# Kernel optimization log

Measured on AMD Instinct MI355X. Metric: run time of the kernel, lower is better.

The kernel has to match this reference:

```python
import jax, jax.numpy as jnp
import numpy as np

C = 512
H_HEADS = 8  # self-attn heads (num_heads) and cross-attn heads (n_heads), both 8


def _self_attn(x, Wq, Wkv):
    # x: [B,N,C]; shared (ModuleParallel) linear weights, qkv_bias=False
    B, N, _ = x.shape
    h, d = H_HEADS, C // H_HEADS
    q = (x @ Wq.T).reshape(B, N, h, d).transpose(0, 2, 1, 3)          # [B,h,N,d]
    kv = (x @ Wkv.T).reshape(B, N, 2, h, d).transpose(2, 0, 3, 1, 4)  # [2,B,h,N,d]
    k, v = kv[0], kv[1]
    attn = jax.nn.softmax(jnp.einsum('bhnd,bhmd->bhnm', q, k) * (d ** -0.5), axis=-1)
    y = jnp.einsum('bhnm,bhmd->bhnd', attn, v).transpose(0, 2, 1, 3).reshape(B, N, C)
    return y


def _judger(y_self, y_other, Wj1, bj1, Wj2, bj2):
    # Mlp_2(2C->C->C) with exact GELU, then softmax over channel dim
    hdn = jax.nn.gelu(jnp.concatenate([y_self, y_other], axis=-1) @ Wj1.T + bj1, approximate=False)
    return jax.nn.softmax(hdn @ Wj2.T + bj2, axis=-1)


def _cross_attn(yq, ykv, kn_row, vn_row, Win, bin_, Wout, bout, rel):
    # Vectorized form of the per-sample loop: each token is a seq-len-1 query
    # attending over 2 keys: [noise_k + yq, yq * relation_score].
    B, N, _ = yq.shape
    h, d = H_HEADS, C // H_HEADS
    qw, kw, vw = Win[:C], Win[C:2 * C], Win[2 * C:]
    bq, bk, bv = bin_[:C], bin_[C:2 * C], bin_[2 * C:]
    k_in = jnp.stack([kn_row + yq, yq * rel], axis=-2)   # [B,N,2,C]
    v_in = jnp.stack([vn_row + yq, ykv], axis=-2)        # [B,N,2,C]
    qp = (yq @ qw.T + bq).reshape(B, N, h, d)
    kp = (k_in @ kw.T + bk).reshape(B, N, 2, h, d)
    vp = (v_in @ vw.T + bv).reshape(B, N, 2, h, d)
    scores = jnp.einsum('bnhd,bnkhd->bnhk', qp, kp) * (d ** -0.5)
    w = jax.nn.softmax(scores, axis=-1)
    o = jnp.einsum('bnhk,bnkhd->bnhd', w, vp).reshape(B, N, C)
    return o @ Wout.T + bout


def setup_inputs() -> dict:
    key = jax.random.key(0)
    ks = jax.random.split(key, 16)
    B, N = 8, 1024
    s = 0.02
    inp = {
        'x0': jax.random.normal(ks[0], (B, N, C), jnp.float32),
        'x1': jax.random.normal(ks[1], (B, N, C), jnp.float32),
        'H': 32, 'W': 32,
        'Wq': jax.random.normal(ks[2], (C, C), jnp.float32) * s,
        'Wkv': jax.random.normal(ks[3], (2 * C, C), jnp.float32) * s,
        'Wj1': jax.random.normal(ks[4], (C, 2 * C), jnp.float32) * s,
        'bj1': jnp.zeros((C,), jnp.float32),
        'Wj2': jax.random.normal(ks[5], (C, C), jnp.float32) * s,
        'bj2': jnp.zeros((C,), jnp.float32),
        'kn': jax.random.normal(ks[6], (2, C), jnp.float32),
        'vn': jax.random.normal(ks[7], (2, C), jnp.float32),
        'Wc0_in': jax.random.normal(ks[8], (3 * C, C), jnp.float32) * s,
        'bc0_in': jnp.zeros((3 * C,), jnp.float32),
        'Wc0_out': jax.random.normal(ks[9], (C, C), jnp.float32) * s,
        'bc0_out': jnp.zeros((C,), jnp.float32),
        'Wc1_in': jax.random.normal(ks[10], (3 * C, C), jnp.float32) * s,
        'bc1_in': jnp.zeros((3 * C,), jnp.float32),
        'Wc1_out': jax.random.normal(ks[11], (C, C), jnp.float32) * s,
        'bc1_out': jnp.zeros((C,), jnp.float32),
        'Wp': jax.random.normal(ks[12], (C, C), jnp.float32) * s,
        'bp': jnp.zeros((C,), jnp.float32),
    }
    return inp


def reference(x0, x1, H, W, Wq, Wkv, Wj1, bj1, Wj2, bj2, kn, vn,
              Wc0_in, bc0_in, Wc0_out, bc0_out, Wc1_in, bc1_in, Wc1_out, bc1_out,
              Wp, bp):
    # Dual self-attention (shared q/kv projections across modalities, sr_ratio=1)
    y0 = _self_attn(x0, Wq, Wkv)
    y1 = _self_attn(x1, Wq, Wkv)
    # Noise-augmented relation-gated cross-attention (vectorized over batch)
    rel0 = _judger(y0, y1, Wj1, bj1, Wj2, bj2)
    rel1 = _judger(y1, y0, Wj1, bj1, Wj2, bj2)
    new0 = y0 + _cross_attn(y0, y1, kn[0], vn[0], Wc0_in, bc0_in, Wc0_out, bc0_out, rel0)
    new1 = y1 + _cross_attn(y1, y0, kn[1], vn[1], Wc1_in, bc1_in, Wc1_out, bc1_out, rel1)
    out0 = new0 @ Wp.T + bp
    out1 = new1 @ Wp.T + bp
    return jnp.stack([out0, out1])  # [2,B,N,C]
```

## Files before the change

kernel.cpp:

```cpp
#include <hip/hip_runtime.h>

typedef unsigned short u16;
typedef u16 u16x8 __attribute__((ext_vector_type(8)));
typedef __bf16 bf16x8 __attribute__((ext_vector_type(8)));
typedef __bf16 bf16x2 __attribute__((ext_vector_type(2)));
typedef float f32x4 __attribute__((ext_vector_type(4)));

__device__ __forceinline__ float b2f(u16 h) {
  union { unsigned u; float f; } x; x.u = ((unsigned)h) << 16; return x.f;
}
__device__ __forceinline__ u16 f2b(float f) {
  union { float f; unsigned u; } x; x.f = f;
  unsigned r = x.u + 0x7FFFu + ((x.u >> 16) & 1u);
  return (u16)(r >> 16);
}
__device__ __forceinline__ f32x4 mfma16(bf16x8 a, bf16x8 b, f32x4 c) {
  return __builtin_amdgcn_mfma_f32_16x16x32_bf16(a, b, c, 0, 0, 0);
}
__device__ __forceinline__ void gload16(const void* g, void* l) {
  __builtin_amdgcn_global_load_lds(
      (const __attribute__((address_space(1))) void*)g,
      (__attribute__((address_space(3))) void*)l, 16, 0, 0);
}
#define WAITV4 asm volatile("s_waitcnt vmcnt(4)" ::: "memory")
#define WAITV0 asm volatile("s_waitcnt vmcnt(0)" ::: "memory")
#define WAITL0 asm volatile("s_waitcnt lgkmcnt(0)" ::: "memory")
#define BARRIER asm volatile("s_barrier" ::: "memory")

__global__ __launch_bounds__(256) void xcvt_k(const float* __restrict__ x0,
                                              const float* __restrict__ x1,
                                              u16* __restrict__ out) {
  int b = blockIdx.x;
  const float* src = (b < 4096) ? x0 : x1;
  u16* dst = out + (b < 4096 ? 0 : 4194304);
  int i = (b & 4095) * 1024 + threadIdx.x * 4;
  float4 v = *(const float4*)&src[i];
  dst[i + 0] = f2b(v.x); dst[i + 1] = f2b(v.y);
  dst[i + 2] = f2b(v.z); dst[i + 3] = f2b(v.w);
}

__global__ __launch_bounds__(256) void wcvt_k(
    const float* __restrict__ wq, const float* __restrict__ wkv,
    const float* __restrict__ wj1, const float* __restrict__ wj2,
    const float* __restrict__ wci0, const float* __restrict__ wci1,
    const float* __restrict__ wp, u16* __restrict__ wsb) {
  int b = blockIdx.x; const float* src; size_t doff; int lb;
  if      (b < 256)  { src = wq;   doff = 0;       lb = b; }
  else if (b < 768)  { src = wkv;  doff = 262144;  lb = b - 256; }
  else if (b < 1280) { src = wj1;  doff = 786432;  lb = b - 768; }
  else if (b < 1536) { src = wj2;  doff = 1310720; lb = b - 1280; }
  else if (b < 2304) { src = wci0; doff = 1572864; lb = b - 1536; }
  else if (b < 3072) { src = wci1; doff = 2359296; lb = b - 2304; }
  else               { src = wp;   doff = 3145728; lb = b - 3072; }
  int i = lb * 1024 + threadIdx.x * 4;
  float4 v = *(const float4*)&src[i];
  u16* dst = wsb + doff + i;
  u16 c0 = f2b(v.x), c1 = f2b(v.y), c2 = f2b(v.z), c3 = f2b(v.w);
  dst[0] = c0; dst[1] = c1; dst[2] = c2; dst[3] = c3;
  if (b >= 3072) {
    int row = i >> 9, col = i & 511;
    u16* f0 = wsb + 3932160 + (size_t)row * 1024 + col;
    u16* f1 = wsb + 4456448 + (size_t)row * 1024 + col;
    f0[0] = c0; f0[1] = c1; f0[2] = c2; f0[3] = c3;
    f1[0] = c0; f1[1] = c1; f1[2] = c2; f1[3] = c3;
  }
}

__global__ __launch_bounds__(256) void tcvt_k(const float* __restrict__ w0,
                                              const float* __restrict__ w1,
                                              u16* __restrict__ o0,
                                              u16* __restrict__ o1) {
  __shared__ u16 t[64][65];
  const int b = blockIdx.x;
  const float* src = (b & 64) ? w1 : w0;
  u16* dst = (b & 64) ? o1 : o0;
  const int r0 = ((b >> 3) & 7) * 64, c0 = (b & 7) * 64;
  const int tid = threadIdx.x;
#pragma unroll
  for (int i = 0; i < 16; i++) {
    int idx = tid + i * 256;
    int r = idx >> 6, c = idx & 63;
    t[r][c] = f2b(src[(size_t)(r0 + r) * 512 + c0 + c]);
  }
  __syncthreads();
#pragma unroll
  for (int i = 0; i < 16; i++) {
    int idx = tid + i * 256;
    int c = idx >> 6, r = idx & 63;
    dst[(size_t)(c0 + c) * 512 + r0 + r] = t[r][c];
  }
}

__global__ __launch_bounds__(256) void cvec_k(
    const float* __restrict__ kn, const float* __restrict__ vn,
    const float* __restrict__ bp, const float* __restrict__ bco0,
    const float* __restrict__ bco1, const u16* __restrict__ wci0,
    const u16* __restrict__ wci1, const u16* __restrict__ wp,
    float* __restrict__ out) {
  int idx = blockIdx.x * 256 + threadIdx.x;
  int which = idx >> 9, col = idx & 511;
  const float* src; const u16* w; float acc;
  if (which < 4) {
    int s = which & 1, isv = which >> 1;
    src = (isv ? vn : kn) + s * 512;
    w = (s ? wci1 : wci0) + (isv ? 524288 : 262144) + (size_t)col * 512;
    acc = 0.f;
  } else {
    int s = which & 1;
    src = s ? bco1 : bco0;
    w = wp + (size_t)col * 512;
    acc = bp[col];
  }
  for (int k = 0; k < 512; k += 8) {
    u16x8 w8 = *(const u16x8*)&w[k];
#pragma unroll
    for (int j = 0; j < 8; j++) acc += src[k + j] * b2f(w8[j]);
  }
  out[idx] = acc;
}

template<int EPI, int AMODE, bool GLA>
__global__ __launch_bounds__(512, 4) void gemm4_k(
    const u16* __restrict__ A, int astr, int K1, int K,
    const u16* __restrict__ W0, const u16* __restrict__ W1,
    const float* __restrict__ b0, const float* __restrict__ b1,
    const u16* __restrict__ mulmat,
    void* __restrict__ outp, int ostr, int ncol) {
  __shared__ u16 SM[32768];
  const int tid = threadIdx.x;
  const int lane = tid & 63;
  const int wv = tid >> 6;
  const int wr = wv >> 1, wc = wv & 1;
  const int lr = lane & 15, lg = lane >> 4;
  const int L = blockIdx.x;
  const int nrow = gridDim.x / ncol;
  int row_b, col_b;
  if ((nrow & 7) == 0) {
    int xcd = L & 7, s = L >> 3;
    row_b = xcd * (nrow >> 3) + s / ncol;
    col_b = s % ncol;
  } else { row_b = L % nrow; col_b = L / nrow; }
  const int row0 = row_b * 128, col0 = col_b * 128;
  const int strm = (row0 >= 8192) ? 1 : 0;
  const u16* W = strm ? W1 : W0;
  const float* bias = strm ? b1 : b0;
  const int shift = (AMODE == 4 && col0 >= 1536) ? 512 : 0;
  const int cxor  = (AMODE == 4 && col0 >= 1536) ? 8192 : 0;
  const int rL = tid >> 3;
  const int bcl = (lane & 7) * 16;

  f32x4 acc[2][4];
#pragma unroll
  for (int m = 0; m < 2; m++)
#pragma unroll
    for (int n = 0; n < 4; n++) acc[m][n] = f32x4{0.f, 0.f, 0.f, 0.f};

  const int nk = K >> 6;

  auto stage = [&](int k0, int buf) {
    const int Ab = buf * 16384, Wb = buf * 16384 + 8192;
#pragma unroll
    for (int ch = 0; ch < 2; ch++) {
      int r = ch * 64 + rL;
      int bcs = bcl ^ ((r & 7) << 4);
      if constexpr (GLA) {
        const char* asrc;
        if constexpr (AMODE == 3) {
          if (k0 < K1)
            asrc = (const char*)(A + (size_t)(row0 + r) * astr) + k0 * 2 + bcs;
          else
            asrc = (const char*)(A + (size_t)((row0 + r) ^ 8192) * astr) +
                   (k0 - K1) * 2 + bcs;
        } else {
          asrc = (const char*)(A + (size_t)((row0 + r) ^ cxor) * astr) +
                 k0 * 2 + bcs;
        }
        gload16(asrc, &SM[Ab + (ch * 64 + wv * 8) * 64]);
      } else {
        int sc = (lane & 7) * 8;
        int kg = k0 + sc;
        u16x8 v = *(const u16x8*)(A + (size_t)(row0 + r) * astr + kg);
        if (AMODE == 2) {
          u16x8 m8 = *(const u16x8*)(mulmat + (size_t)(row0 + r) * K + kg);
#pragma unroll
          for (int j = 0; j < 8; j++) v[j] = f2b(b2f(v[j]) * b2f(m8[j]));
        }
        *(u16x8*)&SM[Ab + r * 64 + (sc ^ ((r & 7) << 3))] = v;
      }
      const char* wsrc =
          (const char*)(W + (size_t)(col0 - shift + r) * K) + k0 * 2 + bcs;
      gload16(wsrc, &SM[Wb + (ch * 64 + wv * 8) * 64]);
    }
  };

  stage(0, 0);
  for (int t = 0; t < nk; t++) {
    const int buf = t & 1;
    if (t + 1 < nk) {
      stage((t + 1) * 64, buf ^ 1);
      if (GLA && AMODE != 2) { WAITV4; } else { WAITV0; }
    } else {
      WAITV0;
    }
    BARRIER;
    const int Ab = buf * 16384, Wb = buf * 16384 + 8192;
#pragma unroll
    for (int kk = 0; kk < 2; kk++) {
      const int c = kk * 32 + lg * 8;
      bf16x8 af[2], wf[4];
#pragma unroll
      for (int m = 0; m < 2; m++) {
        int r = wr * 32 + m * 16 + lr;
        af[m] = *(const bf16x8*)&SM[Ab + r * 64 + (c ^ ((r & 7) << 3))];
      }
#pragma unroll
      for (int n = 0; n < 4; n++) {
        int r = wc * 64 + n * 16 + lr;
        wf[n] = *(const bf16x8*)&SM[Wb + r * 64 + (c ^ ((r & 7) << 3))];
      }
#pragma unroll
      for (int m = 0; m < 2; m++)
#pragma unroll
        for (int n = 0; n < 4; n++)
          acc[m][n] = mfma16(af[m], wf[n], acc[m][n]);
    }
    WAITL0;
    BARRIER;
  }

#pragma unroll
  for (int m = 0; m < 2; m++)
#pragma unroll
    for (int n = 0; n < 4; n++)
#pragma unroll
      for (int r = 0; r < 4; r++) {
        int grow = row0 + wr * 32 + m * 16 + lg * 4 + r;
        int gcol = col0 + wc * 64 + n * 16 + lr;
        float v = acc[m][n][r];
        if (bias) v += bias[gcol - shift];
        if (EPI == 1) v = 0.5f * v * (1.0f + erff(v * 0.70710678118f));
        if (EPI == 3) ((float*)outp)[(size_t)grow * ostr + gcol] = v;
        else          ((u16*)outp)[(size_t)grow * ostr + gcol] = f2b(v);
      }
}

__global__ __launch_bounds__(256) void vtrans_k(const u16* __restrict__ QKV,
                                                u16* __restrict__ VT) {
  __shared__ u16 t[64][66];
  const int tid = threadIdx.x;
  const int bh = blockIdx.y;
  const int sb = bh >> 3, h = bh & 7;
  const int n0 = blockIdx.x * 64;
#pragma unroll
  for (int i = 0; i < 16; i++) {
    int idx = tid + i * 256;
    int r = idx >> 6, c = idx & 63;
    t[r][c] = QKV[((size_t)sb * 1024 + n0 + r) * 1536 + 1024 + h * 64 + c];
  }
  __syncthreads();
#pragma unroll
  for (int i = 0; i < 16; i++) {
    int idx = tid + i * 256;
    int r = idx >> 6, p = idx & 63;
    int tok = ((p >> 5) << 5) + ((p & 31) >> 1) + ((p & 1) << 4);
    VT[((size_t)bh * 64 + r) * 1024 + n0 + p] = t[tok][r];
  }
}

__global__ __launch_bounds__(256) void attn_k(const u16* __restrict__ QKV,
                                              const u16* __restrict__ VT,
                                              u16* __restrict__ OC) {
  __shared__ u16 SM[24576];
  const int STR = 1536;
  const int tid = threadIdx.x, lane = tid & 63, wv = tid >> 6;
  const int lr = lane & 15, lg = lane >> 4;
  const int L = blockIdx.x;
  const int by = L & 127;
  const int q0 = (L >> 7) * 128;
  const int sb = by >> 3, h = by & 7;
  const size_t rowbase = (size_t)sb * 1024;
  const int bcl = (lane & 7) * 16;
  const float SC = 0.18033688f;

  bf16x8 qa[2][2];
#pragma unroll
  for (int m = 0; m < 2; m++)
#pragma unroll
    for (int kk = 0; kk < 2; kk++) {
      int r = q0 + wv * 32 + m * 16 + lr;
      int c = h * 64 + kk * 32 + lg * 8;
      qa[m][kk] = *(const bf16x8*)&QKV[(rowbase + r) * STR + c];
    }

  f32x4 o[2][4];
#pragma unroll
  for (int m = 0; m < 2; m++)
#pragma unroll
    for (int n = 0; n < 4; n++) o[m][n] = f32x4{0.f, 0.f, 0.f, 0.f};
  float ls[2][4] = {{0.f, 0.f, 0.f, 0.f}, {0.f, 0.f, 0.f, 0.f}};

  auto stagekv = [&](int c0, int buf) {
#pragma unroll
    for (int ch = 0; ch < 2; ch++) {
      int r = ch * 32 + (tid >> 3);
      int bcs = bcl ^ ((r & 7) << 4);
      const char* ks =
          (const char*)(QKV + (rowbase + c0 + r) * STR + 512 + h * 64) + bcs;
      gload16(ks, &SM[buf * 8192 + (ch * 32 + wv * 8) * 64]);
      const char* vs =
          (const char*)(VT + ((size_t)by * 64 + r) * 1024 + c0) + bcs;
      gload16(vs, &SM[buf * 8192 + 4096 + (ch * 32 + wv * 8) * 64]);
    }
  };

  stagekv(0, 0);
  for (int t = 0; t < 16; t++) {
    const int buf = t & 1;
    if (t < 15) {
      stagekv((t + 1) * 64, buf ^ 1);
      WAITV4;
    } else {
      WAITV0;
    }
    BARRIER;
    const int Kb = buf * 8192, Vb = buf * 8192 + 4096;

    f32x4 s[2][4];
#pragma unroll
    for (int m = 0; m < 2; m++)
#pragma unroll
      for (int n = 0; n < 4; n++) s[m][n] = f32x4{0.f, 0.f, 0.f, 0.f};
#pragma unroll
    for (int kk = 0; kk < 2; kk++) {
      const int c = kk * 32 + lg * 8;
      bf16x8 kf[4];
#pragma unroll
      for (int n = 0; n < 4; n++) {
        int r = n * 16 + lr;
        kf[n] = *(const bf16x8*)&SM[Kb + r * 64 + (c ^ ((r & 7) << 3))];
      }
#pragma unroll
      for (int m = 0; m < 2; m++)
#pragma unroll
        for (int n = 0; n < 4; n++) s[m][n] = mfma16(qa[m][kk], kf[n], s[m][n]);
    }
#pragma unroll
    for (int m = 0; m < 2; m++)
#pragma unroll
      for (int r = 0; r < 4; r++) {
        int prow = wv * 32 + m * 16 + lg * 4 + r;
        float p00 = __builtin_amdgcn_exp2f(s[m][0][r] * SC);
        float p01 = __builtin_amdgcn_exp2f(s[m][1][r] * SC);
        float p10 = __builtin_amdgcn_exp2f(s[m][2][r] * SC);
        float p11 = __builtin_amdgcn_exp2f(s[m][3][r] * SC);
        ls[m][r] += (p00 + p01) + (p10 + p11);
        bf16x2 w0; w0[0] = (__bf16)p00; w0[1] = (__bf16)p01;
        bf16x2 w1; w1[0] = (__bf16)p10; w1[1] = (__bf16)p11;
        int ib = 16384 + prow * 64, xr = (prow & 7) << 3;
        *(bf16x2*)&SM[ib + ((lr * 2) ^ xr)] = w0;
        *(bf16x2*)&SM[ib + ((32 + lr * 2) ^ xr)] = w1;
      }
#pragma unroll
    for (int kc = 0; kc < 2; kc++) {
      const int cc = kc * 32 + lg * 8;
      bf16x8 pa[2], vf[4];
#pragma unroll
      for (int m = 0; m < 2; m++) {
        int r = wv * 32 + m * 16 + lr;
        pa[m] = *(const bf16x8*)&SM[16384 + r * 64 + (cc ^ ((r & 7) << 3))];
      }
#pragma unroll
      for (int n = 0; n < 4; n++) {
        int r = n * 16 + lr;
        vf[n] = *(const bf16x8*)&SM[Vb + r * 64 + (cc ^ ((r & 7) << 3))];
      }
#pragma unroll
      for (int m = 0; m < 2; m++)
#pragma unroll
        for (int n = 0; n < 4; n++) o[m][n] = mfma16(pa[m], vf[n], o[m][n]);
    }
    WAITL0;
    BARRIER;
  }

#pragma unroll
  for (int m = 0; m < 2; m++)
#pragma unroll
    for (int r = 0; r < 4; r++) {
      float v = ls[m][r];
      v += __shfl_xor(v, 1); v += __shfl_xor(v, 2);
      v += __shfl_xor(v, 4); v += __shfl_xor(v, 8);
      ls[m][r] = v;
    }
#pragma unroll
  for (int m = 0; m < 2; m++)
#pragma unroll
    for (int n = 0; n < 4; n++)
#pragma unroll
      for (int r = 0; r < 4; r++) {
        int grow = q0 + wv * 32 + m * 16 + lg * 4 + r;
        int gcol = h * 64 + n * 16 + lr;
        OC[(rowbase + grow) * 1024 + gcol] = f2b(o[m][n][r] / ls[m][r]);
      }
}

__global__ __launch_bounds__(256) void rsoftmax_k(u16* __restrict__ X) {
  const int row = blockIdx.x * 4 + (threadIdx.x >> 6);
  const int lane = threadIdx.x & 63;
  u16* p = X + (size_t)row * 512 + lane * 8;
  u16x8 v = *(u16x8*)p;
  float e[8]; float s = 0.f;
#pragma unroll
  for (int j = 0; j < 8; j++) { e[j] = __expf(b2f(v[j])); s += e[j]; }
  for (int x = 1; x < 64; x <<= 1) s += __shfl_xor(s, x);
  float inv = 1.0f / s;
#pragma unroll
  for (int j = 0; j < 8; j++) v[j] = f2b(e[j] * inv);
  *(u16x8*)p = v;
}

__global__ __launch_bounds__(256) void twokey3_k(const u16* __restrict__ CP,
                                                 const u16* __restrict__ KP1,
                                                 const float* __restrict__ cvec,
                                                 u16* __restrict__ OC) {
  const int t = blockIdx.x * 4 + (threadIdx.x >> 6);
  const int lane = threadIdx.x & 63;
  const int s = t >> 13;
  const size_t rb = (size_t)t * 2048 + lane * 8;
  u16x8 q8 = *(const u16x8*)&CP[rb];
  u16x8 a8 = *(const u16x8*)&CP[rb + 512];
  u16x8 v0 = *(const u16x8*)&CP[rb + 1024];
  u16x8 v1 = *(const u16x8*)&CP[rb + 1536];
  u16x8 b8 = *(const u16x8*)&KP1[(size_t)t * 512 + lane * 8];
  const float* ck = cvec + s * 512 + lane * 8;
  const float* cv = cvec + 1024 + s * 512 + lane * 8;

  float s0 = 0.f, s1 = 0.f;
#pragma unroll
  for (int j = 0; j < 8; j++) {
    float qf = b2f(q8[j]);
    s0 += qf * (b2f(a8[j]) + ck[j]);
    s1 += qf * b2f(b8[j]);
  }
  s0 += __shfl_xor(s0, 1); s1 += __shfl_xor(s1, 1);
  s0 += __shfl_xor(s0, 2); s1 += __shfl_xor(s1, 2);
  s0 += __shfl_xor(s0, 4); s1 += __shfl_xor(s1, 4);

  float e0 = __expf(s0 * 0.125f), e1 = __expf(s1 * 0.125f);
  float rr = 1.0f / (e0 + e1);
  float w0 = e0 * rr, w1 = e1 * rr;
  u16x8 o8;
#pragma unroll
  for (int j = 0; j < 8; j++)
    o8[j] = f2b(w0 * (b2f(v0[j]) + cv[j]) + w1 * b2f(v1[j]));
  *(u16x8*)&OC[(size_t)t * 1024 + 512 + lane * 8] = o8;
}

extern "C" void kernel_launch(void* const* d_in, const int* in_sizes, int n_in,
                              void* d_out, int out_size, void* d_ws, size_t ws_size,
                              hipStream_t stream) {
  (void)in_sizes; (void)n_in; (void)out_size; (void)ws_size;
  const float* x0  = (const float*)d_in[0];
  const float* x1  = (const float*)d_in[1];
  const float* Wq  = (const float*)d_in[4];
  const float* Wkv = (const float*)d_in[5];
  const float* Wj1 = (const float*)d_in[6];
  const float* bj1 = (const float*)d_in[7];
  const float* Wj2 = (const float*)d_in[8];
  const float* bj2 = (const float*)d_in[9];
  const float* kn  = (const float*)d_in[10];
  const float* vn  = (const float*)d_in[11];
  const float* Wci[2]  = {(const float*)d_in[12], (const float*)d_in[16]};
  const float* bci[2]  = {(const float*)d_in[13], (const float*)d_in[17]};
  const float* Wco[2]  = {(const float*)d_in[14], (const float*)d_in[18]};
  const float* bco[2]  = {(const float*)d_in[15], (const float*)d_in[19]};
  const float* Wp  = (const float*)d_in[20];
  const float* bp  = (const float*)d_in[21];

  u16* wsb = (u16*)d_ws;
  u16* wqb   = wsb;
  u16* wj1b  = wsb + 786432;
  u16* wj2b  = wsb + 1310720;
  u16* wcib[2] = {wsb + 1572864, wsb + 2359296};
  u16* wpb   = wsb + 3145728;
  u16* wcoT[2] = {wsb + 3407872, wsb + 3670016};
  u16* wfin[2] = {wsb + 3932160, wsb + 4456448};
  float* cvecb = (float*)(wsb + 4980736);
  const size_t SLOT = 8388608;
  u16* base = wsb + 5242880;
  u16* S0 = base;
  u16* OC = base + 1 * SLOT;
  u16* S3 = base + 3 * SLOT;
  u16* S4 = base + 4 * SLOT;
  u16* S5 = base + 5 * SLOT;
  u16* S6 = base + 6 * SLOT;
  u16* QKV = S3;
  u16* REL = S3;
  u16* CP  = S3;
  (void)S4; (void)S5;

  dim3 blk(256), gblk(512);
  xcvt_k<<<dim3(8192), blk, 0, stream>>>(x0, x1, S0);
  wcvt_k<<<dim3(3328), blk, 0, stream>>>(Wq, Wkv, Wj1, Wj2, Wci[0], Wci[1],
                                         Wp, wsb);
  tcvt_k<<<dim3(128), blk, 0, stream>>>(Wco[0], Wco[1], wcoT[0], wcoT[1]);
  cvec_k<<<dim3(12), blk, 0, stream>>>(kn, vn, bp, bco[0], bco[1],
                                       wcib[0], wcib[1], wpb, cvecb);
  for (int s = 0; s < 2; s++)
    gemm4_k<0, 0, true><<<dim3(16), gblk, 0, stream>>>(
        wpb, 512, 512, 512, wcoT[s], wcoT[s], nullptr, nullptr, nullptr,
        wfin[s] + 512, 1024, 4);

  gemm4_k<0, 0, true><<<dim3(1536), gblk, 0, stream>>>(
      S0, 512, 512, 512, wqb, wqb, nullptr, nullptr, nullptr, QKV, 1536, 12);
  vtrans_k<<<dim3(16, 128), blk, 0, stream>>>(QKV, S6);
  attn_k<<<dim3(1024), blk, 0, stream>>>(QKV, S6, OC);

  gemm4_k<1, 3, true><<<dim3(512), gblk, 0, stream>>>(
      OC, 1024, 512, 1024, wj1b, wj1b, bj1, bj1, nullptr, S0, 512, 4);
  gemm4_k<0, 0, true><<<dim3(512), gblk, 0, stream>>>(
      S0, 512, 512, 512, wj2b, wj2b, bj2, bj2, nullptr, REL, 512, 4);
  rsoftmax_k<<<dim3(4096), blk, 0, stream>>>(REL);

  gemm4_k<0, 2, false><<<dim3(512), gblk, 0, stream>>>(
      OC, 1024, 512, 512, wcib[0] + 262144, wcib[1] + 262144,
      bci[0] + 512, bci[1] + 512, REL, S0, 512, 4);
  gemm4_k<0, 4, true><<<dim3(2048), gblk, 0, stream>>>(
      OC, 1024, 512, 512, wcib[0], wcib[1], bci[0], bci[1], nullptr,
      CP, 2048, 16);

  twokey3_k<<<dim3(4096), blk, 0, stream>>>(CP, S0, cvecb, OC);

  gemm4_k<3, 0, true><<<dim3(512), gblk, 0, stream>>>(
      OC, 1024, 1024, 1024, wfin[0], wfin[1], cvecb + 2048, cvecb + 2560,
      nullptr, d_out, 512, 4);
}
```

Measured before the change: 316.5 us.

## Restructure GEMM to 4-wave blocks with register-direct A fragments

Replaces the 8-wave GEMM, which staged both A and W tiles through LDS, with a 4-wave kernel. Each wave now computes a 64x64 sub-tile and loads its A fragments straight from global memory into registers, double-buffered in registers, while only W goes through LDS. The softmax of the relation scores is fused with the elementwise multiply by y into a new kernel that writes a separate buffer, so the q/k GEMM no longer does that product inside its A-load path. The cost is more registers per thread and uncoalesced, non-LDS A loads, which could lower occupancy or memory efficiency.

```diff
diff --git a/kernel.cpp b/kernel.cpp
--- a/kernel.cpp
+++ b/kernel.cpp
@@ -119,17 +119,14 @@
   out[idx] = acc;
 }
 
-template<int EPI, int AMODE, bool GLA>
-__global__ __launch_bounds__(512, 4) void gemm4_k(
+template<int EPI, int AMODE>
+__global__ __launch_bounds__(256, 3) void gemm5_k(
     const u16* __restrict__ A, int astr, int K1, int K,
     const u16* __restrict__ W0, const u16* __restrict__ W1,
     const float* __restrict__ b0, const float* __restrict__ b1,
-    const u16* __restrict__ mulmat,
     void* __restrict__ outp, int ostr, int ncol) {
-  __shared__ u16 SM[32768];
-  const int tid = threadIdx.x;
-  const int lane = tid & 63;
-  const int wv = tid >> 6;
+  __shared__ u16 SM[16384];
+  const int tid = threadIdx.x, lane = tid & 63, wv = tid >> 6;
   const int wr = wv >> 1, wc = wv & 1;
   const int lr = lane & 15, lg = lane >> 4;
   const int L = blockIdx.x;
@@ -146,95 +143,84 @@
   const float* bias = strm ? b1 : b0;
   const int shift = (AMODE == 4 && col0 >= 1536) ? 512 : 0;
   const int cxor  = (AMODE == 4 && col0 >= 1536) ? 8192 : 0;
-  const int rL = tid >> 3;
   const int bcl = (lane & 7) * 16;
 
-  f32x4 acc[2][4];
-#pragma unroll
-  for (int m = 0; m < 2; m++)
+  const u16* arow[4];
+#pragma unroll
+  for (int m = 0; m < 4; m++)
+    arow[m] = A + (size_t)((row0 + wr * 64 + m * 16 + lr) ^ cxor) * astr;
+  const long xoff = (AMODE == 3)
+      ? ((row0 < 8192) ? (long)8192 * astr : -(long)8192 * astr) : 0;
+
+  f32x4 acc[4][4];
+#pragma unroll
+  for (int m = 0; m < 4; m++)
 #pragma unroll
     for (int n = 0; n < 4; n++) acc[m][n] = f32x4{0.f, 0.f, 0.f, 0.f};
 
   const int nk = K >> 6;
 
-  auto stage = [&](int k0, int buf) {
-    const int Ab = buf * 16384, Wb = buf * 16384 + 8192;
-#pragma unroll
-    for (int ch = 0; ch < 2; ch++) {
-      int r = ch * 64 + rL;
+  auto stageW = [&](int k0, int buf) {
+#pragma unroll
+    for (int ch = 0; ch < 4; ch++) {
+      int r = ch * 32 + (tid >> 3);
       int bcs = bcl ^ ((r & 7) << 4);
-      if constexpr (GLA) {
-        const char* asrc;
-        if constexpr (AMODE == 3) {
-          if (k0 < K1)
-            asrc = (const char*)(A + (size_t)(row0 + r) * astr) + k0 * 2 + bcs;
-          else
-            asrc = (const char*)(A + (size_t)((row0 + r) ^ 8192) * astr) +
-                   (k0 - K1) * 2 + bcs;
-        } else {
-          asrc = (const char*)(A + (size_t)((row0 + r) ^ cxor) * astr) +
-                 k0 * 2 + bcs;
-        }
-        gload16(asrc, &SM[Ab + (ch * 64 + wv * 8) * 64]);
-      } else {
-        int sc = (lane & 7) * 8;
-        int kg = k0 + sc;
-        u16x8 v = *(const u16x8*)(A + (size_t)(row0 + r) * astr + kg);
-        if (AMODE == 2) {
-          u16x8 m8 = *(const u16x8*)(mulmat + (size_t)(row0 + r) * K + kg);
-#pragma unroll
-          for (int j = 0; j < 8; j++) v[j] = f2b(b2f(v[j]) * b2f(m8[j]));
-        }
-        *(u16x8*)&SM[Ab + r * 64 + (sc ^ ((r & 7) << 3))] = v;
-      }
       const char* wsrc =
           (const char*)(W + (size_t)(col0 - shift + r) * K) + k0 * 2 + bcs;
-      gload16(wsrc, &SM[Wb + (ch * 64 + wv * 8) * 64]);
+      gload16(wsrc, &SM[buf * 8192 + (ch * 32 + wv * 8) * 64]);
     }
   };
-
-  stage(0, 0);
-  for (int t = 0; t < nk; t++) {
-    const int buf = t & 1;
+  auto loadA = [&](bf16x8 (&dst)[4][2], int k0) {
+#pragma unroll
+    for (int m = 0; m < 4; m++) {
+      const u16* ar = (AMODE == 3 && k0 >= K1) ? arow[m] + xoff + (k0 - K1)
+                                               : arow[m] + k0;
+#pragma unroll
+      for (int kk = 0; kk < 2; kk++)
+        dst[m][kk] = *(const bf16x8*)&ar[kk * 32 + lg * 8];
+    }
+  };
+
+  bf16x8 afA[4][2], afB[4][2];
+  stageW(0, 0);
+  loadA(afA, 0);
+
+  auto body = [&](int t, bf16x8 (&cur)[4][2], bf16x8 (&nxt)[4][2]) {
+    WAITV0;
+    BARRIER;
     if (t + 1 < nk) {
-      stage((t + 1) * 64, buf ^ 1);
-      if (GLA && AMODE != 2) { WAITV4; } else { WAITV0; }
-    } else {
-      WAITV0;
-    }
-    BARRIER;
-    const int Ab = buf * 16384, Wb = buf * 16384 + 8192;
+      stageW((t + 1) * 64, (t + 1) & 1);
+      loadA(nxt, (t + 1) * 64);
+    }
+    const int Wb = (t & 1) * 8192;
 #pragma unroll
     for (int kk = 0; kk < 2; kk++) {
       const int c = kk * 32 + lg * 8;
-      bf16x8 af[2], wf[4];
-#pragma unroll
-      for (int m = 0; m < 2; m++) {
-        int r = wr * 32 + m * 16 + lr;
-        af[m] = *(const bf16x8*)&SM[Ab + r * 64 + (c ^ ((r & 7) << 3))];
-      }
+      bf16x8 wf[4];
 #pragma unroll
       for (int n = 0; n < 4; n++) {
         int r = wc * 64 + n * 16 + lr;
         wf[n] = *(const bf16x8*)&SM[Wb + r * 64 + (c ^ ((r & 7) << 3))];
       }
 #pragma unroll
-      for (int m = 0; m < 2; m++)
+      for (int m = 0; m < 4; m++)
 #pragma unroll
         for (int n = 0; n < 4; n++)
-          acc[m][n] = mfma16(af[m], wf[n], acc[m][n]);
-    }
-    WAITL0;
-    BARRIER;
-  }
-
-#pragma unroll
-  for (int m = 0; m < 2; m++)
+          acc[m][n] = mfma16(cur[m][kk], wf[n], acc[m][n]);
+    }
+  };
+  for (int t = 0; t < nk; t += 2) {
+    body(t, afA, afB);
+    body(t + 1, afB, afA);
+  }
+
+#pragma unroll
+  for (int m = 0; m < 4; m++)
 #pragma unroll
     for (int n = 0; n < 4; n++)
 #pragma unroll
       for (int r = 0; r < 4; r++) {
-        int grow = row0 + wr * 32 + m * 16 + lg * 4 + r;
+        int grow = row0 + wr * 64 + m * 16 + lg * 4 + r;
         int gcol = col0 + wc * 64 + n * 16 + lr;
         float v = acc[m][n][r];
         if (bias) v += bias[gcol - shift];
@@ -404,19 +390,22 @@
       }
 }
 
-__global__ __launch_bounds__(256) void rsoftmax_k(u16* __restrict__ X) {
+__global__ __launch_bounds__(256) void relmul_k(const u16* __restrict__ RL,
+                                                const u16* __restrict__ OC,
+                                                u16* __restrict__ YKR) {
   const int row = blockIdx.x * 4 + (threadIdx.x >> 6);
   const int lane = threadIdx.x & 63;
-  u16* p = X + (size_t)row * 512 + lane * 8;
-  u16x8 v = *(u16x8*)p;
+  u16x8 lv = *(const u16x8*)&RL[(size_t)row * 512 + lane * 8];
   float e[8]; float s = 0.f;
 #pragma unroll
-  for (int j = 0; j < 8; j++) { e[j] = __expf(b2f(v[j])); s += e[j]; }
+  for (int j = 0; j < 8; j++) { e[j] = __expf(b2f(lv[j])); s += e[j]; }
   for (int x = 1; x < 64; x <<= 1) s += __shfl_xor(s, x);
   float inv = 1.0f / s;
-#pragma unroll
-  for (int j = 0; j < 8; j++) v[j] = f2b(e[j] * inv);
-  *(u16x8*)p = v;
+  u16x8 y8 = *(const u16x8*)&OC[(size_t)row * 1024 + lane * 8];
+  u16x8 o8;
+#pragma unroll
+  for (int j = 0; j < 8; j++) o8[j] = f2b(b2f(y8[j]) * (e[j] * inv));
+  *(u16x8*)&YKR[(size_t)row * 512 + lane * 8] = o8;
 }
 
 __global__ __launch_bounds__(256) void twokey3_k(const u16* __restrict__ CP,
@@ -492,14 +481,13 @@
   u16* OC = base + 1 * SLOT;
   u16* S3 = base + 3 * SLOT;
   u16* S4 = base + 4 * SLOT;
-  u16* S5 = base + 5 * SLOT;
   u16* S6 = base + 6 * SLOT;
   u16* QKV = S3;
   u16* REL = S3;
   u16* CP  = S3;
-  (void)S4; (void)S5;
-
-  dim3 blk(256), gblk(512);
+  u16* YKR = S4;
+
+  dim3 blk(256);
   xcvt_k<<<dim3(8192), blk, 0, stream>>>(x0, x1, S0);
   wcvt_k<<<dim3(3328), blk, 0, stream>>>(Wq, Wkv, Wj1, Wj2, Wci[0], Wci[1],
                                          Wp, wsb);
@@ -507,31 +495,29 @@
   cvec_k<<<dim3(12), blk, 0, stream>>>(kn, vn, bp, bco[0], bco[1],
                                        wcib[0], wcib[1], wpb, cvecb);
   for (int s = 0; s < 2; s++)
-    gemm4_k<0, 0, true><<<dim3(16), gblk, 0, stream>>>(
-        wpb, 512, 512, 512, wcoT[s], wcoT[s], nullptr, nullptr, nullptr,
+    gemm5_k<0, 0><<<dim3(16), blk, 0, stream>>>(
+        wpb, 512, 512, 512, wcoT[s], wcoT[s], nullptr, nullptr,
         wfin[s] + 512, 1024, 4);
 
-  gemm4_k<0, 0, true><<<dim3(1536), gblk, 0, stream>>>(
-      S0, 512, 512, 512, wqb, wqb, nullptr, nullptr, nullptr, QKV, 1536, 12);
+  gemm5_k<0, 0><<<dim3(1536), blk, 0, stream>>>(
+      S0, 512, 512, 512, wqb, wqb, nullptr, nullptr, QKV, 1536, 12);
   vtrans_k<<<dim3(16, 128), blk, 0, stream>>>(QKV, S6);
   attn_k<<<dim3(1024), blk, 0, stream>>>(QKV, S6, OC);
 
-  gemm4_k<1, 3, true><<<dim3(512), gblk, 0, stream>>>(
-      OC, 1024, 512, 1024, wj1b, wj1b, bj1, bj1, nullptr, S0, 512, 4);
-  gemm4_k<0, 0, true><<<dim3(512), gblk, 0, stream>>>(
-      S0, 512, 512, 512, wj2b, wj2b, bj2, bj2, nullptr, REL, 512, 4);
-  rsoftmax_k<<<dim3(4096), blk, 0, stream>>>(REL);
-
-  gemm4_k<0, 2, false><<<dim3(512), gblk, 0, stream>>>(
-      OC, 1024, 512, 512, wcib[0] + 262144, wcib[1] + 262144,
-      bci[0] + 512, bci[1] + 512, REL, S0, 512, 4);
-  gemm4_k<0, 4, true><<<dim3(2048), gblk, 0, stream>>>(
-      OC, 1024, 512, 512, wcib[0], wcib[1], bci[0], bci[1], nullptr,
-      CP, 2048, 16);
+  gemm5_k<1, 3><<<dim3(512), blk, 0, stream>>>(
+      OC, 1024, 512, 1024, wj1b, wj1b, bj1, bj1, S0, 512, 4);
+  gemm5_k<0, 0><<<dim3(512), blk, 0, stream>>>(
+      S0, 512, 512, 512, wj2b, wj2b, bj2, bj2, REL, 512, 4);
+  relmul_k<<<dim3(4096), blk, 0, stream>>>(REL, OC, YKR);
+  gemm5_k<0, 0><<<dim3(512), blk, 0, stream>>>(
+      YKR, 512, 512, 512, wcib[0] + 262144, wcib[1] + 262144,
+      bci[0] + 512, bci[1] + 512, S0, 512, 4);
+  gemm5_k<0, 4><<<dim3(2048), blk, 0, stream>>>(
+      OC, 1024, 512, 512, wcib[0], wcib[1], bci[0], bci[1], CP, 2048, 16);
 
   twokey3_k<<<dim3(4096), blk, 0, stream>>>(CP, S0, cvecb, OC);
 
-  gemm4_k<3, 0, true><<<dim3(512), gblk, 0, stream>>>(
+  gemm5_k<3, 0><<<dim3(512), blk, 0, stream>>>(
       OC, 1024, 1024, 1024, wfin[0], wfin[1], cvecb + 2048, cvecb + 2560,
-      nullptr, d_out, 512, 4);
-}
+      d_out, 512, 4);
+}
```

Result: slower. 633.7 us (+100.2%).
